# Kernel optimization log

Measured on AMD Instinct MI355X. Metric: run time of the kernel, lower is better.

## Reference

```python
import jax, jax.numpy as jnp
import numpy as np

HEADS = 8
TQ, QH, QW = 4, 16, 16
TK, KH, KW = 4, 16, 16
DIM = 64


def setup_inputs() -> dict:
    key = jax.random.key(0)
    k1, k2, k3, k4, k5 = jax.random.split(key, 5)
    return {
        "query": jax.random.normal(k1, (4, HEADS, TQ * QH * QW, DIM), dtype=jnp.float32),
        "scores": jax.random.normal(k2, (4, HEADS, TQ * QH * QW, TK * KH * KW), dtype=jnp.float32),
        "height_embeddings": jax.random.normal(k3, (2 * (max(QH, KH) - 1) + 1, DIM), dtype=jnp.float32),
        "width_embeddings": jax.random.normal(k4, (2 * (max(QW, KW) - 1) + 1, DIM), dtype=jnp.float32),
        "time_embeddings": jax.random.normal(k5, (2 * (max(TQ, TK) - 1) + 1, DIM), dtype=jnp.float32),
    }


def _rel_dist(q_n, k_n):
    # matches torch: ratios are both 1 when q_n == k_n
    q_ratio = round(max(k_n / q_n, 1.0))
    k_ratio = round(max(q_n / k_n, 1.0))
    d = jnp.arange(q_n)[:, None] * q_ratio - jnp.arange(k_n)[None, :] * k_ratio
    return d + (k_n - 1) * k_ratio  # [q_n, k_n] int indices


def reference(query, scores, height_embeddings, width_embeddings, time_embeddings):
    Rh = height_embeddings[_rel_dist(QH, KH)]  # [QH, KH, DIM]
    Rw = width_embeddings[_rel_dist(QW, KW)]   # [QW, KW, DIM]
    Rt = time_embeddings[_rel_dist(TQ, TK)]    # [TQ, TK, DIM]

    q = query.reshape(-1, HEADS, TQ, QH, QW, DIM)
    rel_h = jnp.einsum('bNthwc,hkc->bNthwk', q, Rh)  # [B,N,T,H,W,KH]
    rel_w = jnp.einsum('bNthwc,wkc->bNthwk', q, Rw)  # [B,N,T,H,W,KW]
    rel_t = jnp.einsum('bNthwc,tkc->bNthwk', q, Rt)  # [B,N,T,H,W,TK]

    s = scores.reshape(-1, HEADS, TQ, QH, QW, TK, KH, KW)
    s = (s
         + rel_h[:, :, :, :, :, None, :, None]
         + rel_w[:, :, :, :, :, None, None, :]
         + rel_t[:, :, :, :, :, :, None, None])
    return s.reshape(-1, HEADS, TQ * QH * QW, TK * KH * KW)
```

## Files before the change

kernel.cpp:

```cpp
#include <hip/hip_runtime.h>

#define NHEADS 8
#define TQ 4
#define QH 16
#define QW 16
#define TK 4
#define KH 16
#define KW 16
#define DIM 64
#define BATCH 4

__global__ __launch_bounds__(256) void relpos_kernel(
    const float* __restrict__ query,
    const float* __restrict__ scores,
    const float* __restrict__ hemb,
    const float* __restrict__ wemb,
    const float* __restrict__ temb,
    float* __restrict__ out)
{
    const int tid  = threadIdx.x;
    const int row0 = blockIdx.x << 2;
    const int pos  = row0 & 1023;
    const int t  = pos >> 8;
    const int h  = (pos >> 4) & 15;
    const int w0 = pos & 15;

    const float4* sc4 = (const float4*)(scores + (size_t)row0 * 1024);
    float4 s0 = sc4[tid];
    float4 s1 = sc4[256 + tid];
    float4 s2 = sc4[512 + tid];
    float4 s3 = sc4[768 + tid];

    __shared__ float rel[4][36];

    if (tid < 144) {
        const int r = tid / 36;
        const int j = tid - r * 36;
        const float* emb;
        int e;
        if (j < 16)      { emb = hemb; e = h - j + 15; }
        else if (j < 32) { emb = wemb; e = (w0 + r) - (j - 16) + 15; }
        else             { emb = temb; e = t - (j - 32) + 3; }
        const float4* e4 = (const float4*)(emb + (size_t)e * DIM);
        const float4* q4 = (const float4*)(query + (size_t)(row0 + r) * DIM);
        float acc = 0.f;
#pragma unroll
        for (int c = 0; c < DIM / 4; ++c) {
            float4 qv = q4[c];
            float4 ev = e4[c];
            acc += qv.x * ev.x + qv.y * ev.y + qv.z * ev.z + qv.w * ev.w;
        }
        rel[r][j] = acc;
    }
    __syncthreads();

    const int base = tid << 2;
    const int tk  = base >> 8;
    const int kh  = (base >> 4) & 15;
    const int kw0 = base & 15;

    float4* o4 = (float4*)(out + (size_t)row0 * 1024);
#pragma unroll
    for (int r = 0; r < 4; ++r) {
        const float4 s = (r == 0) ? s0 : (r == 1) ? s1 : (r == 2) ? s2 : s3;
        const float a = rel[r][kh] + rel[r][32 + tk];
        float4 o;
        o.x = s.x + a + rel[r][16 + kw0 + 0];
        o.y = s.y + a + rel[r][16 + kw0 + 1];
        o.z = s.z + a + rel[r][16 + kw0 + 2];
        o.w = s.w + a + rel[r][16 + kw0 + 3];
        o4[r * 256 + tid] = o;
    }
}

extern "C" void kernel_launch(void* const* d_in, const int* in_sizes, int n_in,
                              void* d_out, int out_size, void* d_ws, size_t ws_size,
                              hipStream_t stream) {
    const float* query  = (const float*)d_in[0];
    const float* scores = (const float*)d_in[1];
    const float* hemb   = (const float*)d_in[2];
    const float* wemb   = (const float*)d_in[3];
    const float* temb   = (const float*)d_in[4];
    float* out = (float*)d_out;

    const int rows = BATCH * NHEADS * TQ * QH * QW;
    relpos_kernel<<<dim3(rows / 4), dim3(256), 0, stream>>>(query, scores, hemb, wemb, temb, out);
}
```

Measured before the change: 251.0 us.

## Split bias dot products into a separate kernel and grid-stride stream the score add

Precomputes the per-row relative-position dot products into a workspace buffer with a dedicated kernel, then runs a pure streaming kernel that reads scores, gathers bias terms from the buffer and writes output using a fixed grid with several independent loads in flight per thread. This removes the dot-product prologue and block-wide barrier from the bandwidth-bound path. It adds a second launch and an extra small buffer round trip, and falls back to the old fused kernel if the workspace is too small.

```diff
diff --git a/kernel.cpp b/kernel.cpp
--- a/kernel.cpp
+++ b/kernel.cpp
@@ -10,13 +10,91 @@
 #define DIM 64
 #define BATCH 4
 
-__global__ __launch_bounds__(256) void relpos_kernel(
+#define ROWS (BATCH * NHEADS * TQ * QH * QW)
+#define RELSTRIDE 40
+
+__global__ __launch_bounds__(256) void bias_kernel(
     const float* __restrict__ query,
-    const float* __restrict__ scores,
     const float* __restrict__ hemb,
     const float* __restrict__ wemb,
     const float* __restrict__ temb,
+    float* __restrict__ relbuf)
+{
+    const int g = blockIdx.x * 256 + threadIdx.x;
+    if (g >= ROWS * 36) return;
+    const int row = g / 36;
+    const int j = g - row * 36;
+
+    const int pos = row & 1023;
+    const int t = pos >> 8;
+    const int h = (pos >> 4) & 15;
+    const int w = pos & 15;
+
+    const float* emb;
+    int e;
+    if (j < 16)      { emb = hemb; e = h - j + 15; }
+    else if (j < 32) { emb = wemb; e = w - (j - 16) + 15; }
+    else             { emb = temb; e = t - (j - 32) + 3; }
+
+    const float4* e4 = (const float4*)(emb + (size_t)e * DIM);
+    const float4* q4 = (const float4*)(query + (size_t)row * DIM);
+    float acc = 0.f;
+#pragma unroll
+    for (int c = 0; c < DIM / 4; ++c) {
+        float4 qv = q4[c];
+        float4 ev = e4[c];
+        acc += qv.x * ev.x + qv.y * ev.y + qv.z * ev.z + qv.w * ev.w;
+    }
+    relbuf[(size_t)row * RELSTRIDE + j] = acc;
+}
+
+#define BBLOCKS 2048
+__global__ __launch_bounds__(256) void stream_kernel(
+    const float* __restrict__ scores,
+    const float* __restrict__ relbuf,
     float* __restrict__ out)
+{
+    const int total4 = ROWS * 256;
+    const int stride = BBLOCKS * 256;
+    const float4* sc4 = (const float4*)scores;
+    float4* o4 = (float4*)out;
+
+    int f0 = blockIdx.x * 256 + threadIdx.x;
+#pragma unroll
+    for (int i = 0; i < 4; ++i) {
+        int f[4];
+        float4 s[4], wv[4];
+        float a[4];
+#pragma unroll
+        for (int k = 0; k < 4; ++k) {
+            f[k] = f0 + (4 * i + k) * stride;
+            const int sub = f[k] & 255;
+            const int row = f[k] >> 8;
+            const int tk  = sub >> 6;
+            const int kh  = (sub >> 2) & 15;
+            const int kw0 = (sub & 3) << 2;
+            const float* rel = relbuf + (size_t)row * RELSTRIDE;
+            s[k]  = sc4[f[k]];
+            wv[k] = *(const float4*)(rel + 16 + kw0);
+            a[k]  = rel[kh] + rel[32 + tk];
+        }
+#pragma unroll
+        for (int k = 0; k < 4; ++k) {
+            float4 o;
+            o.x = s[k].x + a[k] + wv[k].x;
+            o.y = s[k].y + a[k] + wv[k].y;
+            o.z = s[k].z + a[k] + wv[k].z;
+            o.w = s[k].w + a[k] + wv[k].w;
+            o4[f[k]] = o;
+        }
+    }
+    (void)total4;
+}
+
+__global__ __launch_bounds__(256) void relpos_fallback(
+    const float* __restrict__ query, const float* __restrict__ scores,
+    const float* __restrict__ hemb, const float* __restrict__ wemb,
+    const float* __restrict__ temb, float* __restrict__ out)
 {
     const int tid  = threadIdx.x;
     const int row0 = blockIdx.x << 2;
@@ -26,18 +104,13 @@
     const int w0 = pos & 15;
 
     const float4* sc4 = (const float4*)(scores + (size_t)row0 * 1024);
-    float4 s0 = sc4[tid];
-    float4 s1 = sc4[256 + tid];
-    float4 s2 = sc4[512 + tid];
-    float4 s3 = sc4[768 + tid];
+    float4 s0 = sc4[tid], s1 = sc4[256 + tid], s2 = sc4[512 + tid], s3 = sc4[768 + tid];
 
     __shared__ float rel[4][36];
-
     if (tid < 144) {
         const int r = tid / 36;
         const int j = tid - r * 36;
-        const float* emb;
-        int e;
+        const float* emb; int e;
         if (j < 16)      { emb = hemb; e = h - j + 15; }
         else if (j < 32) { emb = wemb; e = (w0 + r) - (j - 16) + 15; }
         else             { emb = temb; e = t - (j - 32) + 3; }
@@ -46,8 +119,7 @@
         float acc = 0.f;
 #pragma unroll
         for (int c = 0; c < DIM / 4; ++c) {
-            float4 qv = q4[c];
-            float4 ev = e4[c];
+            float4 qv = q4[c]; float4 ev = e4[c];
             acc += qv.x * ev.x + qv.y * ev.y + qv.z * ev.z + qv.w * ev.w;
         }
         rel[r][j] = acc;
@@ -55,10 +127,7 @@
     __syncthreads();
 
     const int base = tid << 2;
-    const int tk  = base >> 8;
-    const int kh  = (base >> 4) & 15;
-    const int kw0 = base & 15;
-
+    const int tk = base >> 8, kh = (base >> 4) & 15, kw0 = base & 15;
     float4* o4 = (float4*)(out + (size_t)row0 * 1024);
 #pragma unroll
     for (int r = 0; r < 4; ++r) {
@@ -83,6 +152,15 @@
     const float* temb   = (const float*)d_in[4];
     float* out = (float*)d_out;
 
-    const int rows = BATCH * NHEADS * TQ * QH * QW;
-    relpos_kernel<<<dim3(rows / 4), dim3(256), 0, stream>>>(query, scores, hemb, wemb, temb, out);
+    const size_t need = (size_t)ROWS * RELSTRIDE * sizeof(float);
+    if (ws_size >= need) {
+        float* relbuf = (float*)d_ws;
+        const int adots = ROWS * 36;
+        bias_kernel<<<dim3((adots + 255) / 256), dim3(256), 0, stream>>>(
+            query, hemb, wemb, temb, relbuf);
+        stream_kernel<<<dim3(BBLOCKS), dim3(256), 0, stream>>>(scores, relbuf, out);
+    } else {
+        relpos_fallback<<<dim3(ROWS / 4), dim3(256), 0, stream>>>(
+            query, scores, hemb, wemb, temb, out);
+    }
 }
```

After: 293.0 us. 1.17x slower.
